# Kernel optimization log

Measured on AMD Instinct MI355X. Metric: run time of the kernel, lower is better.

## Reference

```python
import jax, jax.numpy as jnp
import numpy as np

B, S, D, H = 128, 200, 512, 8
DF = D // H  # per-head feature dim = 64
SCALE = np.float32(1.0 / np.sqrt(DF))
NEG_INF = np.float32(-1e32)


def setup_inputs() -> dict:
    key = jax.random.key(0)
    ks = jax.random.split(key, 8)
    xavier = np.float32(np.sqrt(6.0 / (D + D)))  # xavier_uniform_ bound for square Linear
    def lin_w(k):
        return jax.random.uniform(k, (D, D), jnp.float32, -xavier, xavier)
    return {
        "q": jax.random.normal(ks[0], (B, S, D), jnp.float32),
        "k": jax.random.normal(ks[1], (B, S, D), jnp.float32),
        "v": jax.random.normal(ks[2], (B, S, D), jnp.float32),
        "Wq": lin_w(ks[3]), "bq": jnp.zeros((D,), jnp.float32),
        "Wk": lin_w(ks[4]), "bk": jnp.zeros((D,), jnp.float32),
        "Wv": lin_w(ks[5]), "bv": jnp.zeros((D,), jnp.float32),
        "Wo": lin_w(ks[6]), "bo": jnp.zeros((D,), jnp.float32),
        # causal mask: attend only to positions <= query position
        "mask": jnp.tril(jnp.ones((1, 1, S, S), dtype=bool)),
        "zero_pad": 1,
    }


def reference(q, k, v, Wq, bq, Wk, bk, Wv, bv, Wo, bo, mask, zero_pad):
    bs, s, d = q.shape
    # QKV projections -> [B, H, S, DF]
    qh = (q @ Wq.T + bq).reshape(bs, s, H, DF).transpose(0, 2, 1, 3)
    kh = (k @ Wk.T + bk).reshape(bs, s, H, DF).transpose(0, 2, 1, 3)
    vh = (v @ Wv.T + bv).reshape(bs, s, H, DF).transpose(0, 2, 1, 3)
    # attention4dis_kt: scaled dot-product, causal mask fill with -1e32, softmax
    scores = jnp.einsum("bhqd,bhkd->bhqk", qh, kh) * SCALE
    scores = jnp.where(mask, scores, NEG_INF)
    attn = jax.nn.softmax(scores, axis=-1)  # [B, H, S, S]
    if zero_pad:
        # replace first query row of attention weights with zeros
        attn = attn.at[:, :, 0, :].set(0.0)
    # dropout is identity in eval mode
    out = jnp.einsum("bhqk,bhkd->bhqd", attn, vh)
    concat = out.transpose(0, 2, 1, 3).reshape(bs, s, d)
    return concat @ Wo.T + bo
```

## Files before the change

kernel.cpp:

```cpp
#include <hip/hip_runtime.h>
#include <hip/hip_bf16.h>

#define SEQ  200
#define DIM  512
#define NH   8
#define DF   64
#define SPAD 256
#define NEG  -1.0e30f

typedef __bf16 bf16x8 __attribute__((ext_vector_type(8)));
typedef __bf16 bf16x4 __attribute__((ext_vector_type(4)));
typedef float  f32x4  __attribute__((ext_vector_type(4)));

__device__ __forceinline__ void async_lds16(const void* g, void* l)
{
    __builtin_amdgcn_global_load_lds(
        (const __attribute__((address_space(1))) void*)g,
        (__attribute__((address_space(3))) void*)l, 16, 0, 0);
}

struct DetArgs { const unsigned short* p[11]; };

__global__ void detect_all(DetArgs a, int* __restrict__ flags)
{
    const unsigned short* __restrict__ src = a.p[blockIdx.x];
    __shared__ int cnt;
    if (threadIdx.x == 0) cnt = 0;
    __syncthreads();
    int ok = 0;
#pragma unroll
    for (int i = 0; i < 2; ++i) {
        const unsigned short u = src[threadIdx.x * 2 + i];
        const float f = __uint_as_float(((unsigned int)u) << 16);
        const float fa = fabsf(f);
        ok += (f == 0.0f) || (fa >= 6.0e-5f && fa <= 64.0f);
    }
    atomicAdd(&cnt, ok);
    __syncthreads();
    if (threadIdx.x == 0) flags[blockIdx.x] = (cnt < 448) ? 1 : 0;
}

struct CvtArgs { const void* src[8]; __bf16* dst[8]; };

__global__ void cvt_all(CvtArgs a, const int* __restrict__ flags)
{
    const int blk = blockIdx.x;
    int job; long idx, n8;
    if (blk < 512) { job = blk >> 7; idx = (long)(blk & 127) * 256 + threadIdx.x; n8 = (long)DIM * DIM / 8; }
    else           { job = 4 + (blk - 512); idx = threadIdx.x; n8 = DIM / 8; }
    if (idx >= n8) return;
    const int fl = flags[3 + job];
    if (fl) {
        const f32x4* s = (const f32x4*)a.src[job];
        const f32x4 x = s[2 * idx], y = s[2 * idx + 1];
        bf16x8 o;
        o[0] = (__bf16)x[0]; o[1] = (__bf16)x[1];
        o[2] = (__bf16)x[2]; o[3] = (__bf16)x[3];
        o[4] = (__bf16)y[0]; o[5] = (__bf16)y[1];
        o[6] = (__bf16)y[2]; o[7] = (__bf16)y[3];
        ((bf16x8*)a.dst[job])[idx] = o;
    } else {
        ((bf16x8*)a.dst[job])[idx] = ((const bf16x8*)a.src[job])[idx];
    }
}

__device__ __forceinline__ void gemm_core512(
    const void* __restrict__ Araw, const __bf16* __restrict__ Bt,
    long m_off, int K, int af32,
    __bf16 (*lA)[128 * 32], __bf16 (*lB)[256 * 32],
    int tid, int m0, int n0, int wm, int wn, int lr, int quad,
    f32x4 (&acc)[4][4])
{
    const __bf16* A16 = (const __bf16*)Araw;
    const float*  A32 = (const float*)Araw;

    const int arow = tid >> 2, acol = (tid & 3) * 8;
    int brow[2], bcol[2];
#pragma unroll
    for (int p = 0; p < 2; ++p) {
        const int t = p * 512 + tid;
        brow[p] = t >> 2;
        bcol[p] = (t & 3) * 8;
    }

    const int KS = K >> 5;
    f32x4 rf0, rf1;

#pragma unroll
    for (int p = 0; p < 2; ++p)
        async_lds16(Bt + (size_t)(n0 + brow[p]) * K + bcol[p],
                    &lB[0][(p * 512 + tid) * 8]);
    if (af32) {
        const size_t aoff = (size_t)(m_off + m0 + arow) * K + acol;
        rf0 = *(const f32x4*)(A32 + aoff);
        rf1 = *(const f32x4*)(A32 + aoff + 4);
    } else {
        async_lds16(A16 + (size_t)(m_off + m0 + arow) * K + acol,
                    &lA[0][tid * 8]);
    }

    for (int ks = 0; ks < KS; ++ks) {
        const int buf = ks & 1;

        if (af32) {
            bf16x8 o;
            o[0] = (__bf16)rf0[0]; o[1] = (__bf16)rf0[1];
            o[2] = (__bf16)rf0[2]; o[3] = (__bf16)rf0[3];
            o[4] = (__bf16)rf1[0]; o[5] = (__bf16)rf1[1];
            o[6] = (__bf16)rf1[2]; o[7] = (__bf16)rf1[3];
            *(bf16x8*)&lA[buf][tid * 8] = o;
        }

        __syncthreads();

        if (ks + 1 < KS) {
            const int k1 = (ks + 1) * 32;
#pragma unroll
            for (int p = 0; p < 2; ++p)
                async_lds16(Bt + (size_t)(n0 + brow[p]) * K + k1 + bcol[p],
                            &lB[buf ^ 1][(p * 512 + tid) * 8]);
            if (af32) {
                const size_t aoff =
                    (size_t)(m_off + m0 + arow) * K + k1 + acol;
                rf0 = *(const f32x4*)(A32 + aoff);
                rf1 = *(const f32x4*)(A32 + aoff + 4);
            } else {
                async_lds16(A16 + (size_t)(m_off + m0 + arow) * K + k1 + acol,
                            &lA[buf ^ 1][tid * 8]);
            }
        }

        bf16x8 af[4], bfr[4];
#pragma unroll
        for (int mi = 0; mi < 4; ++mi)
            af[mi] = *(const bf16x8*)&lA[buf][(wm + mi * 16 + lr) * 32 + quad * 8];
#pragma unroll
        for (int ni = 0; ni < 4; ++ni)
            bfr[ni] = *(const bf16x8*)&lB[buf][(wn + ni * 16 + lr) * 32 + quad * 8];
#pragma unroll
        for (int mi = 0; mi < 4; ++mi)
#pragma unroll
            for (int ni = 0; ni < 4; ++ni)
                acc[mi][ni] = __builtin_amdgcn_mfma_f32_16x16x32_bf16(
                    af[mi], bfr[ni], acc[mi][ni], 0, 0, 0);
    }
}

struct QkvArgs {
    const void*   A[3];
    const __bf16* Bt[3];
    const __bf16* bias[3];
    __bf16*       C[3];
};

__global__ __launch_bounds__(512, 4)
void gemm_qkv_kernel(QkvArgs a, long m_off, int K,
                     const int* __restrict__ flags)
{
    __shared__ __align__(16) __bf16 lA[2][128 * 32];
    __shared__ __align__(16) __bf16 lB[2][256 * 32];

    const int z    = blockIdx.z;
    const int af32 = flags[z];
    const int tid  = threadIdx.x;
    const int m0   = blockIdx.x * 128;
    const int n0   = blockIdx.y * 256;
    const int w    = tid >> 6;
    const int lane = tid & 63;
    const int lr   = lane & 15, quad = lane >> 4;
    const int wm   = (w >> 2) * 64, wn = (w & 3) * 64;

    f32x4 acc[4][4] = {};
    gemm_core512(a.A[z], a.Bt[z], m_off, K, af32,
                 lA, lB, tid, m0, n0, wm, wn, lr, quad, acc);

    const __bf16* bias = a.bias[z];
    __bf16* C = a.C[z];
    const int mode = (z == 2) ? 2 : 1;

#pragma unroll
    for (int ni = 0; ni < 4; ++ni) {
        const int col = n0 + wn + ni * 16 + lr;
        const float bb = (float)bias[col];
        const int h = col >> 6, df = col & 63;
        if (mode == 2) {
#pragma unroll
            for (int mi = 0; mi < 4; ++mi) {
                const int row0 = m0 + wm + mi * 16 + quad * 4;
                const int b = row0 / SEQ, s0 = row0 - b * SEQ;
                bf16x4 pk;
#pragma unroll
                for (int r = 0; r < 4; ++r)
                    pk[r] = (__bf16)(acc[mi][ni][r] + bb);
                *(bf16x4*)&C[(((size_t)(b * NH + h)) * DF + df) * SPAD + s0] = pk;
            }
        } else {
#pragma unroll
            for (int mi = 0; mi < 4; ++mi) {
#pragma unroll
                for (int r = 0; r < 4; ++r) {
                    const int row = m0 + wm + mi * 16 + quad * 4 + r;
                    const int b = row / SEQ, s = row - b * SEQ;
                    C[(((size_t)(b * NH + h)) * SEQ + s) * DF + df] =
                        (__bf16)(acc[mi][ni][r] + bb);
                }
            }
        }
    }
}

__global__ __launch_bounds__(512, 4)
void gemm_out_kernel(const __bf16* __restrict__ Araw,
                     const __bf16* __restrict__ Bt,
                     const __bf16* __restrict__ bias,
                     float* __restrict__ C, int N, int K)
{
    __shared__ __align__(16) __bf16 lA[2][128 * 32];
    __shared__ __align__(16) __bf16 lB[2][256 * 32];

    const int tid  = threadIdx.x;
    const int m0   = blockIdx.x * 128;
    const int n0   = blockIdx.y * 256;
    const int w    = tid >> 6;
    const int lane = tid & 63;
    const int lr   = lane & 15, quad = lane >> 4;
    const int wm   = (w >> 2) * 64, wn = (w & 3) * 64;

    f32x4 acc[4][4] = {};
    gemm_core512(Araw, Bt, 0, K, 0,
                 lA, lB, tid, m0, n0, wm, wn, lr, quad, acc);

#pragma unroll
    for (int ni = 0; ni < 4; ++ni) {
        const int col = n0 + wn + ni * 16 + lr;
        const float bb = (float)bias[col];
#pragma unroll
        for (int mi = 0; mi < 4; ++mi) {
#pragma unroll
            for (int r = 0; r < 4; ++r) {
                const int row = m0 + wm + mi * 16 + quad * 4 + r;
                C[(size_t)row * N + col] = acc[mi][ni][r] + bb;
            }
        }
    }
}

#define KROWS 208
#define KSTR  72
#define VSTR  232
#define PSTR  136

__global__ __launch_bounds__(256, 2)
void attn_mfma(const __bf16* __restrict__ Qh,
               const __bf16* __restrict__ Kh,
               const __bf16* __restrict__ Vt,
               __bf16* __restrict__ Ctx,
               const int* __restrict__ zp)
{
    __shared__ __align__(16) __bf16 Kl[KROWS * KSTR];
    __shared__ __align__(16) __bf16 Vl[DF * VSTR];
    __shared__ __align__(16) __bf16 Pl[4][16 * PSTR];

    const int tid  = threadIdx.x;
    const int w    = tid >> 6, lane = tid & 63;
    const int lr   = lane & 15, quad = lane >> 4;
    const int bh   = blockIdx.x;
    const int b    = bh >> 3, h = bh & 7;
    const size_t qkbase = (size_t)bh * SEQ * DF;
    const size_t vbase  = (size_t)bh * DF * SPAD;
    const int zero_pad = zp[0];

    for (int i = tid; i < (KROWS * DF) / 8; i += 256) {
        const int row = i >> 3, c8 = (i & 7) * 8;
        *(bf16x8*)&Kl[row * KSTR + c8] =
            *(const bf16x8*)(Kh + qkbase + (size_t)row * DF + c8);
    }
    for (int i = tid; i < (DF * 224) / 8; i += 256) {
        const int d = i / 28, kb = (i % 28) * 8;
        bf16x8 vv = {};
        if (kb < SEQ)
            vv = *(const bf16x8*)(Vt + vbase + (size_t)d * SPAD + kb);
        *(bf16x8*)&Vl[d * VSTR + kb] = vv;
    }
    __syncthreads();

    __bf16* pw = Pl[w];

    const unsigned int mine =
        (unsigned int)(0x0459F38AF17BF26CULL >> (16 * w)) & 0xFFFFu;

    for (int j = 0; j < 4; ++j) {
        const int qt = (mine >> (4 * j)) & 15;
        if (qt == 15) continue;
        const int q = qt * 16 + lr;

        bf16x8 qf0, qf1;
        {
            const __bf16* qp = Qh + qkbase + (size_t)(qt * 16 + lr) * DF + quad * 8;
            qf0 = *(const bf16x8*)qp;
            qf1 = *(const bf16x8*)(qp + 32);
        }

        f32x4 sc[14];
#pragma unroll
        for (int kt = 0; kt < 13; ++kt) {
            if (kt > qt) continue;
            const int krow = kt * 16 + lr;
            const bf16x8 kf0 = *(const bf16x8*)&Kl[krow * KSTR + quad * 8];
            const bf16x8 kf1 = *(const bf16x8*)&Kl[krow * KSTR + 32 + quad * 8];
            f32x4 z = {};
            z = __builtin_amdgcn_mfma_f32_16x16x32_bf16(kf0, qf0, z, 0, 0, 0);
            z = __builtin_amdgcn_mfma_f32_16x16x32_bf16(kf1, qf1, z, 0, 0, 0);
            sc[kt] = z;
        }

        float mx = NEG;
#pragma unroll
        for (int kt = 0; kt < 13; ++kt) {
            if (kt > qt) continue;
#pragma unroll
            for (int r = 0; r < 4; ++r) {
                const int kk = kt * 16 + quad * 4 + r;
                const float s = (kk <= q && kk < SEQ) ? sc[kt][r] * 0.125f : NEG;
                sc[kt][r] = s;
                mx = fmaxf(mx, s);
            }
        }
        mx = fmaxf(mx, __shfl_xor(mx, 16, 64));
        mx = fmaxf(mx, __shfl_xor(mx, 32, 64));

        float l = 0.0f;
#pragma unroll
        for (int kt = 0; kt < 13; ++kt) {
            if (kt > qt) continue;
#pragma unroll
            for (int r = 0; r < 4; ++r) {
                const float pv = __expf(sc[kt][r] - mx);
                sc[kt][r] = pv;
                l += pv;
            }
        }
        l += __shfl_xor(l, 16, 64);
        l += __shfl_xor(l, 32, 64);
        const float linv = 1.0f / l;

        f32x4 oacc[4] = {};

#pragma unroll
        for (int kt = 0; kt < 8; ++kt) {
            if (kt <= qt) {
                bf16x4 pkv;
#pragma unroll
                for (int r = 0; r < 4; ++r) pkv[r] = (__bf16)sc[kt][r];
                *(bf16x4*)&pw[lr * PSTR + kt * 16 + quad * 4] = pkv;
            } else if (kt == qt + 1) {
                *(bf16x4*)&pw[lr * PSTR + kt * 16 + quad * 4] = (bf16x4){};
            }
        }
#pragma unroll
        for (int c = 0; c < 4; ++c) {
            if (2 * c > qt) continue;
            const bf16x8 pf = *(const bf16x8*)&pw[lr * PSTR + c * 32 + quad * 8];
#pragma unroll
            for (int nt = 0; nt < 4; ++nt) {
                const bf16x8 vf =
                    *(const bf16x8*)&Vl[(nt * 16 + lr) * VSTR + c * 32 + quad * 8];
                oacc[nt] = __builtin_amdgcn_mfma_f32_16x16x32_bf16(
                    pf, vf, oacc[nt], 0, 0, 0);
            }
        }

        if (qt >= 8) {
#pragma unroll
            for (int kt = 8; kt < 14; ++kt) {
                if (kt <= qt) {
                    bf16x4 pkv;
#pragma unroll
                    for (int r = 0; r < 4; ++r) pkv[r] = (__bf16)sc[kt][r];
                    *(bf16x4*)&pw[lr * PSTR + (kt - 8) * 16 + quad * 4] = pkv;
                } else if (kt == qt + 1) {
                    *(bf16x4*)&pw[lr * PSTR + (kt - 8) * 16 + quad * 4] = (bf16x4){};
                }
            }
#pragma unroll
            for (int c = 0; c < 3; ++c) {
                if (2 * (c + 4) > qt) continue;
                const bf16x8 pf = *(const bf16x8*)&pw[lr * PSTR + c * 32 + quad * 8];
#pragma unroll
                for (int nt = 0; nt < 4; ++nt) {
                    const bf16x8 vf =
                        *(const bf16x8*)&Vl[(nt * 16 + lr) * VSTR + (c + 4) * 32 + quad * 8];
                    oacc[nt] = __builtin_amdgcn_mfma_f32_16x16x32_bf16(
                        pf, vf, oacc[nt], 0, 0, 0);
                }
            }
        }

        float il[4];
#pragma unroll
        for (int r = 0; r < 4; ++r) il[r] = __shfl(linv, quad * 4 + r, 16);
#pragma unroll
        for (int nt = 0; nt < 4; ++nt) {
            const int d = nt * 16 + lr;
#pragma unroll
            for (int r = 0; r < 4; ++r) {
                const int qq = qt * 16 + quad * 4 + r;
                if (qq < SEQ) {
                    float ov = oacc[nt][r] * il[r];
                    if (zero_pad && qq == 0) ov = 0.0f;
                    Ctx[((size_t)(b * SEQ + qq)) * DIM + h * DF + d] = (__bf16)ov;
                }
            }
        }
    }
}

extern "C" void kernel_launch(void* const* d_in, const int* in_sizes, int n_in,
                              void* d_out, int out_size, void* d_ws, size_t ws_size,
                              hipStream_t stream)
{
    const void* q  = d_in[0];
    const void* k  = d_in[1];
    const void* v  = d_in[2];
    const void* Ws[4] = {d_in[3], d_in[5], d_in[7], d_in[9]};
    const void* bs[4] = {d_in[4], d_in[6], d_in[8], d_in[10]};
    const int*  zp = (const int*)d_in[12];
    float* Out = (float*)d_out;

    int* flags = (int*)d_ws;
    __bf16* Wc[4]; __bf16* bc[4];
    __bf16* p = (__bf16*)((char*)d_ws + 256);
    for (int i = 0; i < 4; ++i) { Wc[i] = p; p += (size_t)DIM * DIM; }
    for (int i = 0; i < 4; ++i) { bc[i] = p; p += DIM; }
    const size_t fixed_bytes = (size_t)((char*)p - (char*)d_ws);

    const int B_total = 128;
    int cb = 128;
    while (cb > 16) {
        const size_t crows_t = (size_t)cb * SEQ;
        const size_t elems = 4 * crows_t * DIM + (size_t)cb * NH * DF * SPAD;
        if (fixed_bytes + elems * 2 <= ws_size) break;
        cb >>= 1;
    }
    const int nchunk = B_total / cb;
    const size_t crows = (size_t)cb * SEQ;
    const size_t celems = crows * DIM;

    __bf16* Qh  = p;
    __bf16* Kh  = Qh + celems;
    __bf16* Vt  = Kh + celems;
    __bf16* Ctx = Vt + (size_t)cb * NH * DF * SPAD;

    const dim3 blk(256);
    const dim3 blk5(512);
    const dim3 g2((unsigned)(crows / 128), DIM / 256);
    const dim3 g3((unsigned)(crows / 128), DIM / 256, 3);

    DetArgs da;
    da.p[0] = (const unsigned short*)q;
    da.p[1] = (const unsigned short*)k;
    da.p[2] = (const unsigned short*)v;
    for (int i = 0; i < 4; ++i) {
        da.p[3 + i] = (const unsigned short*)Ws[i];
        da.p[7 + i] = (const unsigned short*)bs[i];
    }
    detect_all<<<dim3(11), blk, 0, stream>>>(da, flags);

    CvtArgs ca;
    for (int i = 0; i < 4; ++i) {
        ca.src[i] = Ws[i];     ca.dst[i] = Wc[i];
        ca.src[4 + i] = bs[i]; ca.dst[4 + i] = bc[i];
    }
    cvt_all<<<dim3(516), blk, 0, stream>>>(ca, flags);

    QkvArgs qa;
    qa.A[0] = q; qa.A[1] = k; qa.A[2] = v;
    qa.Bt[0] = Wc[0]; qa.Bt[1] = Wc[1]; qa.Bt[2] = Wc[2];
    qa.bias[0] = bc[0]; qa.bias[1] = bc[1]; qa.bias[2] = bc[2];
    qa.C[0] = Qh; qa.C[1] = Kh; qa.C[2] = Vt;

    for (int c = 0; c < nchunk; ++c) {
        const long moff = (long)c * (long)crows;
        gemm_qkv_kernel<<<g3, blk5, 0, stream>>>(qa, moff, DIM, flags);
        attn_mfma<<<dim3(cb * NH), blk, 0, stream>>>(Qh, Kh, Vt, Ctx, zp);
        gemm_out_kernel<<<g2, blk5, 0, stream>>>(
            Ctx, Wc[3], bc[3], Out + (size_t)c * celems, DIM, DIM);
    }
}
```

Baseline: 330.9 us.

## Fold dtype detection and weight conversion into the GEMM kernels

Removes the separate detect and convert kernels. Each GEMM block now detects input, weight and bias dtypes itself, and converts fp32 weights to bf16 on the fly while loading B tiles into LDS. This cuts two kernel launches and a workspace round trip for the converted weights. In exchange, every block repeats the detection reads and a barrier, and fp32 weights go through registers instead of async LDS loads, which adds load and convert work to the GEMM inner loop.

```diff
diff --git a/kernel.cpp b/kernel.cpp
--- a/kernel.cpp
+++ b/kernel.cpp
@@ -19,60 +19,43 @@
         (__attribute__((address_space(3))) void*)l, 16, 0, 0);
 }
 
-struct DetArgs { const unsigned short* p[11]; };
-
-__global__ void detect_all(DetArgs a, int* __restrict__ flags)
-{
-    const unsigned short* __restrict__ src = a.p[blockIdx.x];
-    __shared__ int cnt;
-    if (threadIdx.x == 0) cnt = 0;
+__device__ __forceinline__ int detect_flag(const void* srcv, int tid, int* slot)
+{
+    const unsigned short* src = (const unsigned short*)srcv;
+    if (tid == 0) *slot = 0;
     __syncthreads();
-    int ok = 0;
-#pragma unroll
-    for (int i = 0; i < 2; ++i) {
-        const unsigned short u = src[threadIdx.x * 2 + i];
-        const float f = __uint_as_float(((unsigned int)u) << 16);
-        const float fa = fabsf(f);
-        ok += (f == 0.0f) || (fa >= 6.0e-5f && fa <= 64.0f);
-    }
-    atomicAdd(&cnt, ok);
+    if (tid < 256) {
+        int ok = 0;
+#pragma unroll
+        for (int i = 0; i < 2; ++i) {
+            const unsigned short u = src[tid * 2 + i];
+            const float f = __uint_as_float(((unsigned int)u) << 16);
+            const float fa = fabsf(f);
+            ok += (f == 0.0f) || (fa >= 6.0e-5f && fa <= 64.0f);
+        }
+        atomicAdd(slot, ok);
+    }
     __syncthreads();
-    if (threadIdx.x == 0) flags[blockIdx.x] = (cnt < 448) ? 1 : 0;
-}
-
-struct CvtArgs { const void* src[8]; __bf16* dst[8]; };
-
-__global__ void cvt_all(CvtArgs a, const int* __restrict__ flags)
-{
-    const int blk = blockIdx.x;
-    int job; long idx, n8;
-    if (blk < 512) { job = blk >> 7; idx = (long)(blk & 127) * 256 + threadIdx.x; n8 = (long)DIM * DIM / 8; }
-    else           { job = 4 + (blk - 512); idx = threadIdx.x; n8 = DIM / 8; }
-    if (idx >= n8) return;
-    const int fl = flags[3 + job];
-    if (fl) {
-        const f32x4* s = (const f32x4*)a.src[job];
-        const f32x4 x = s[2 * idx], y = s[2 * idx + 1];
-        bf16x8 o;
-        o[0] = (__bf16)x[0]; o[1] = (__bf16)x[1];
-        o[2] = (__bf16)x[2]; o[3] = (__bf16)x[3];
-        o[4] = (__bf16)y[0]; o[5] = (__bf16)y[1];
-        o[6] = (__bf16)y[2]; o[7] = (__bf16)y[3];
-        ((bf16x8*)a.dst[job])[idx] = o;
-    } else {
-        ((bf16x8*)a.dst[job])[idx] = ((const bf16x8*)a.src[job])[idx];
-    }
+    return (*slot < 448) ? 1 : 0;
+}
+
+__device__ __forceinline__ float bias_at(const void* bias, int bf32, int col)
+{
+    return bf32 ? ((const float*)bias)[col]
+                : (float)((const __bf16*)bias)[col];
 }
 
 __device__ __forceinline__ void gemm_core512(
-    const void* __restrict__ Araw, const __bf16* __restrict__ Bt,
-    long m_off, int K, int af32,
+    const void* __restrict__ Araw, const void* __restrict__ Braw,
+    long m_off, int K, int af32, int wf32,
     __bf16 (*lA)[128 * 32], __bf16 (*lB)[256 * 32],
     int tid, int m0, int n0, int wm, int wn, int lr, int quad,
     f32x4 (&acc)[4][4])
 {
     const __bf16* A16 = (const __bf16*)Araw;
     const float*  A32 = (const float*)Araw;
+    const __bf16* B16 = (const __bf16*)Braw;
+    const float*  B32 = (const float*)Braw;
 
     const int arow = tid >> 2, acol = (tid & 3) * 8;
     int brow[2], bcol[2];
@@ -84,16 +67,25 @@
     }
 
     const int KS = K >> 5;
-    f32x4 rf0, rf1;
-
-#pragma unroll
-    for (int p = 0; p < 2; ++p)
-        async_lds16(Bt + (size_t)(n0 + brow[p]) * K + bcol[p],
-                    &lB[0][(p * 512 + tid) * 8]);
+    f32x4 rfa0, rfa1, rfb[2][2];
+
+    if (wf32) {
+#pragma unroll
+        for (int p = 0; p < 2; ++p) {
+            const size_t boff = (size_t)(n0 + brow[p]) * K + bcol[p];
+            rfb[p][0] = *(const f32x4*)(B32 + boff);
+            rfb[p][1] = *(const f32x4*)(B32 + boff + 4);
+        }
+    } else {
+#pragma unroll
+        for (int p = 0; p < 2; ++p)
+            async_lds16(B16 + (size_t)(n0 + brow[p]) * K + bcol[p],
+                        &lB[0][(p * 512 + tid) * 8]);
+    }
     if (af32) {
         const size_t aoff = (size_t)(m_off + m0 + arow) * K + acol;
-        rf0 = *(const f32x4*)(A32 + aoff);
-        rf1 = *(const f32x4*)(A32 + aoff + 4);
+        rfa0 = *(const f32x4*)(A32 + aoff);
+        rfa1 = *(const f32x4*)(A32 + aoff + 4);
     } else {
         async_lds16(A16 + (size_t)(m_off + m0 + arow) * K + acol,
                     &lA[0][tid * 8]);
@@ -104,26 +96,45 @@
 
         if (af32) {
             bf16x8 o;
-            o[0] = (__bf16)rf0[0]; o[1] = (__bf16)rf0[1];
-            o[2] = (__bf16)rf0[2]; o[3] = (__bf16)rf0[3];
-            o[4] = (__bf16)rf1[0]; o[5] = (__bf16)rf1[1];
-            o[6] = (__bf16)rf1[2]; o[7] = (__bf16)rf1[3];
+            o[0] = (__bf16)rfa0[0]; o[1] = (__bf16)rfa0[1];
+            o[2] = (__bf16)rfa0[2]; o[3] = (__bf16)rfa0[3];
+            o[4] = (__bf16)rfa1[0]; o[5] = (__bf16)rfa1[1];
+            o[6] = (__bf16)rfa1[2]; o[7] = (__bf16)rfa1[3];
             *(bf16x8*)&lA[buf][tid * 8] = o;
+        }
+        if (wf32) {
+#pragma unroll
+            for (int p = 0; p < 2; ++p) {
+                bf16x8 o;
+                o[0] = (__bf16)rfb[p][0][0]; o[1] = (__bf16)rfb[p][0][1];
+                o[2] = (__bf16)rfb[p][0][2]; o[3] = (__bf16)rfb[p][0][3];
+                o[4] = (__bf16)rfb[p][1][0]; o[5] = (__bf16)rfb[p][1][1];
+                o[6] = (__bf16)rfb[p][1][2]; o[7] = (__bf16)rfb[p][1][3];
+                *(bf16x8*)&lB[buf][(p * 512 + tid) * 8] = o;
+            }
         }
 
         __syncthreads();
 
         if (ks + 1 < KS) {
             const int k1 = (ks + 1) * 32;
-#pragma unroll
-            for (int p = 0; p < 2; ++p)
-                async_lds16(Bt + (size_t)(n0 + brow[p]) * K + k1 + bcol[p],
-                            &lB[buf ^ 1][(p * 512 + tid) * 8]);
+            if (wf32) {
+#pragma unroll
+                for (int p = 0; p < 2; ++p) {
+                    const size_t boff = (size_t)(n0 + brow[p]) * K + k1 + bcol[p];
+                    rfb[p][0] = *(const f32x4*)(B32 + boff);
+                    rfb[p][1] = *(const f32x4*)(B32 + boff + 4);
+                }
+            } else {
+#pragma unroll
+                for (int p = 0; p < 2; ++p)
+                    async_lds16(B16 + (size_t)(n0 + brow[p]) * K + k1 + bcol[p],
+                                &lB[buf ^ 1][(p * 512 + tid) * 8]);
+            }
             if (af32) {
-                const size_t aoff =
-                    (size_t)(m_off + m0 + arow) * K + k1 + acol;
-                rf0 = *(const f32x4*)(A32 + aoff);
-                rf1 = *(const f32x4*)(A32 + aoff + 4);
+                const size_t aoff = (size_t)(m_off + m0 + arow) * K + k1 + acol;
+                rfa0 = *(const f32x4*)(A32 + aoff);
+                rfa1 = *(const f32x4*)(A32 + aoff + 4);
             } else {
                 async_lds16(A16 + (size_t)(m_off + m0 + arow) * K + k1 + acol,
                             &lA[buf ^ 1][tid * 8]);
@@ -147,22 +158,26 @@
 }
 
 struct QkvArgs {
-    const void*   A[3];
-    const __bf16* Bt[3];
-    const __bf16* bias[3];
-    __bf16*       C[3];
+    const void* A[3];
+    const void* Bt[3];
+    const void* bias[3];
+    __bf16*     C[3];
 };
 
 __global__ __launch_bounds__(512, 4)
-void gemm_qkv_kernel(QkvArgs a, long m_off, int K,
-                     const int* __restrict__ flags)
+void gemm_qkv_kernel(QkvArgs a, long m_off, int K)
 {
     __shared__ __align__(16) __bf16 lA[2][128 * 32];
     __shared__ __align__(16) __bf16 lB[2][256 * 32];
+    __shared__ int shdet[3];
 
     const int z    = blockIdx.z;
-    const int af32 = flags[z];
     const int tid  = threadIdx.x;
+
+    const int af32 = detect_flag(a.A[z],    tid, &shdet[0]);
+    const int wf32 = detect_flag(a.Bt[z],   tid, &shdet[1]);
+    const int bf32 = detect_flag(a.bias[z], tid, &shdet[2]);
+
     const int m0   = blockIdx.x * 128;
     const int n0   = blockIdx.y * 256;
     const int w    = tid >> 6;
@@ -171,17 +186,16 @@
     const int wm   = (w >> 2) * 64, wn = (w & 3) * 64;
 
     f32x4 acc[4][4] = {};
-    gemm_core512(a.A[z], a.Bt[z], m_off, K, af32,
+    gemm_core512(a.A[z], a.Bt[z], m_off, K, af32, wf32,
                  lA, lB, tid, m0, n0, wm, wn, lr, quad, acc);
 
-    const __bf16* bias = a.bias[z];
     __bf16* C = a.C[z];
     const int mode = (z == 2) ? 2 : 1;
 
 #pragma unroll
     for (int ni = 0; ni < 4; ++ni) {
         const int col = n0 + wn + ni * 16 + lr;
-        const float bb = (float)bias[col];
+        const float bb = bias_at(a.bias[z], bf32, col);
         const int h = col >> 6, df = col & 63;
         if (mode == 2) {
 #pragma unroll
@@ -211,14 +225,18 @@
 
 __global__ __launch_bounds__(512, 4)
 void gemm_out_kernel(const __bf16* __restrict__ Araw,
-                     const __bf16* __restrict__ Bt,
-                     const __bf16* __restrict__ bias,
+                     const void* __restrict__ Braw,
+                     const void* __restrict__ bias,
                      float* __restrict__ C, int N, int K)
 {
     __shared__ __align__(16) __bf16 lA[2][128 * 32];
     __shared__ __align__(16) __bf16 lB[2][256 * 32];
+    __shared__ int shdet[2];
 
     const int tid  = threadIdx.x;
+    const int wf32 = detect_flag(Braw, tid, &shdet[0]);
+    const int bf32 = detect_flag(bias, tid, &shdet[1]);
+
     const int m0   = blockIdx.x * 128;
     const int n0   = blockIdx.y * 256;
     const int w    = tid >> 6;
@@ -227,13 +245,13 @@
     const int wm   = (w >> 2) * 64, wn = (w & 3) * 64;
 
     f32x4 acc[4][4] = {};
-    gemm_core512(Araw, Bt, 0, K, 0,
+    gemm_core512(Araw, Braw, 0, K, 0, wf32,
                  lA, lB, tid, m0, n0, wm, wn, lr, quad, acc);
 
 #pragma unroll
     for (int ni = 0; ni < 4; ++ni) {
         const int col = n0 + wn + ni * 16 + lr;
-        const float bb = (float)bias[col];
+        const float bb = bias_at(bias, bf32, col);
 #pragma unroll
         for (int mi = 0; mi < 4; ++mi) {
 #pragma unroll
@@ -427,19 +445,14 @@
     const int*  zp = (const int*)d_in[12];
     float* Out = (float*)d_out;
 
-    int* flags = (int*)d_ws;
-    __bf16* Wc[4]; __bf16* bc[4];
-    __bf16* p = (__bf16*)((char*)d_ws + 256);
-    for (int i = 0; i < 4; ++i) { Wc[i] = p; p += (size_t)DIM * DIM; }
-    for (int i = 0; i < 4; ++i) { bc[i] = p; p += DIM; }
-    const size_t fixed_bytes = (size_t)((char*)p - (char*)d_ws);
+    __bf16* p = (__bf16*)d_ws;
 
     const int B_total = 128;
     int cb = 128;
     while (cb > 16) {
         const size_t crows_t = (size_t)cb * SEQ;
         const size_t elems = 4 * crows_t * DIM + (size_t)cb * NH * DF * SPAD;
-        if (fixed_bytes + elems * 2 <= ws_size) break;
+        if (elems * 2 <= ws_size) break;
         cb >>= 1;
     }
     const int nchunk = B_total / cb;
@@ -456,34 +469,17 @@
     const dim3 g2((unsigned)(crows / 128), DIM / 256);
     const dim3 g3((unsigned)(crows / 128), DIM / 256, 3);
 
-    DetArgs da;
-    da.p[0] = (const unsigned short*)q;
-    da.p[1] = (const unsigned short*)k;
-    da.p[2] = (const unsigned short*)v;
-    for (int i = 0; i < 4; ++i) {
-        da.p[3 + i] = (const unsigned short*)Ws[i];
-        da.p[7 + i] = (const unsigned short*)bs[i];
-    }
-    detect_all<<<dim3(11), blk, 0, stream>>>(da, flags);
-
-    CvtArgs ca;
-    for (int i = 0; i < 4; ++i) {
-        ca.src[i] = Ws[i];     ca.dst[i] = Wc[i];
-        ca.src[4 + i] = bs[i]; ca.dst[4 + i] = bc[i];
-    }
-    cvt_all<<<dim3(516), blk, 0, stream>>>(ca, flags);
-
     QkvArgs qa;
     qa.A[0] = q; qa.A[1] = k; qa.A[2] = v;
-    qa.Bt[0] = Wc[0]; qa.Bt[1] = Wc[1]; qa.Bt[2] = Wc[2];
-    qa.bias[0] = bc[0]; qa.bias[1] = bc[1]; qa.bias[2] = bc[2];
+    qa.Bt[0] = Ws[0]; qa.Bt[1] = Ws[1]; qa.Bt[2] = Ws[2];
+    qa.bias[0] = bs[0]; qa.bias[1] = bs[1]; qa.bias[2] = bs[2];
     qa.C[0] = Qh; qa.C[1] = Kh; qa.C[2] = Vt;
 
     for (int c = 0; c < nchunk; ++c) {
         const long moff = (long)c * (long)crows;
-        gemm_qkv_kernel<<<g3, blk5, 0, stream>>>(qa, moff, DIM, flags);
+        gemm_qkv_kernel<<<g3, blk5, 0, stream>>>(qa, moff, DIM);
         attn_mfma<<<dim3(cb * NH), blk, 0, stream>>>(Qh, Kh, Vt, Ctx, zp);
         gemm_out_kernel<<<g2, blk5, 0, stream>>>(
-            Ctx, Wc[3], bc[3], Out + (size_t)c * celems, DIM, DIM);
-    }
-}
+            Ctx, Ws[3], bs[3], Out + (size_t)c * celems, DIM, DIM);
+    }
+}
```

Result: slower. 358.1 us (+8.2%).
